# Performance work log

Measured on AMD Instinct MI355X. Metric: run time of the kernel, lower is better.

Reference implementation:

```python
import jax, jax.numpy as jnp
import numpy as np

TOKENS = 512
DIM_HEAD = 64
MAX_TOKENS = 2000
HEADS = 8
BATCH = 8


def _build_indices(tokens: int, max_tokens: int) -> np.ndarray:
    # Faithful replication of the torch index construction (done once in numpy).
    idx = np.arange(-tokens, tokens + 1)
    pad = max_tokens - 2 * tokens + 1
    row = np.concatenate([np.full(pad, idx[0]), idx, np.full(pad, idx[-1])])
    mat = np.stack([np.roll(row, i) for i in range(max_tokens)])
    mat = mat[: max_tokens - tokens + 2, max_tokens - tokens + 1 :]
    # torch fancy indexing wraps negative indices -> take mod of table size
    return (mat % (2 * tokens - 1)).astype(np.int32)


def setup_inputs() -> dict:
    key = jax.random.key(0)
    kq, kp = jax.random.split(key)
    scale = DIM_HEAD ** (-0.5)
    q = jax.random.normal(kq, (BATCH, HEADS, TOKENS, DIM_HEAD), dtype=jnp.float32)
    rel_pos_emb = (
        jax.random.normal(kp, (HEADS, 2 * TOKENS - 1, DIM_HEAD), dtype=jnp.float32)
        * scale
    )
    indices = jnp.asarray(_build_indices(TOKENS, MAX_TOKENS))
    return {"q": q, "rel_pos_emb": rel_pos_emb, "indices": indices}


def reference(q, rel_pos_emb, indices):
    t = q.shape[2]
    idx = indices[:t, :t]  # [r, t]
    # gather: [heads, r, t, dim_head]
    gathered = rel_pos_emb[:, idx]
    # emb[b,h,t,r] = sum_d q[b,h,t,d] * gathered[h,r,t,d]
    return jnp.einsum("bhtd,hrtd->bhtr", q, gathered)
```

## Files before the change

kernel.cpp:

```cpp
#include <hip/hip_runtime.h>


#define TOKENS 512
#define DIMH 64
#define NREL 1023
#define IDXN 1490

#define ESTR 72
#define PSTR 17
#define PCOLS 80

typedef short bf16x8 __attribute__((ext_vector_type(8)));
typedef float f32x4 __attribute__((ext_vector_type(4)));

__device__ __forceinline__ unsigned short f2bf(float x) {
    unsigned u = __float_as_uint(x);
    return (unsigned short)((u + 0x7FFFu + ((u >> 16) & 1u)) >> 16);
}
__device__ __forceinline__ bf16x8 cvt8(float4 a, float4 b) {
    bf16x8 r;
    r[0] = (short)f2bf(a.x); r[1] = (short)f2bf(a.y);
    r[2] = (short)f2bf(a.z); r[3] = (short)f2bf(a.w);
    r[4] = (short)f2bf(b.x); r[5] = (short)f2bf(b.y);
    r[6] = (short)f2bf(b.z); r[7] = (short)f2bf(b.w);
    return r;
}

__global__ __launch_bounds__(256, 4)
void relpos_wave(const float* __restrict__ q,
                 const float* __restrict__ emb,
                 const int* __restrict__ indices,
                 float* __restrict__ out)
{
    __shared__ unsigned short Es[128 * ESTR];
    __shared__ float Ps[4 * PCOLS * PSTR];

    const int tid = threadIdx.x;
    const int blk = blockIdx.x;
    const int rt = blk & 7;
    const int tt = (blk >> 3) & 7;
    const int bh = blk >> 6;
    const int h  = bh & 7;
    const int t0 = tt * 64;
    const int r0 = rt * 64;

    const int j_a = indices[(size_t)(r0 + 63) * IDXN + t0];

    const int lane = tid & 63;
    const int wave = tid >> 6;
    const int quad = lane >> 4;
    const int l15  = lane & 15;

    {
        const float* embh = emb + (size_t)h * NREL * DIMH;
        const int c16 = tid & 15;
        const int rbase = tid >> 4;
#pragma unroll
        for (int it = 0; it < 8; ++it) {
            const int row = rbase + it * 16;
            int j = j_a + row;
            if (j >= NREL) j -= NREL;
            const float4 v = *(const float4*)(embh + (size_t)j * DIMH + c16 * 4);
            ushort4 w = { f2bf(v.x), f2bf(v.y), f2bf(v.z), f2bf(v.w) };
            *(ushort4*)(Es + (size_t)row * ESTR + c16 * 4) = w;
        }
    }

    bf16x8 af0, af1;
    {
        const float* qp = q + ((size_t)bh * TOKENS + t0 + wave * 16 + l15) * DIMH
                        + quad * 8;
        float4 a0 = *(const float4*)qp;
        float4 a1 = *(const float4*)(qp + 4);
        float4 c0 = *(const float4*)(qp + 32);
        float4 c1 = *(const float4*)(qp + 36);
        af0 = cvt8(a0, a1);
        af1 = cvt8(c0, c1);
    }

    __syncthreads();

    float* psw = Ps + (size_t)wave * (PCOLS * PSTR);

#pragma unroll
    for (int i = 0; i < 5; ++i) {
        const unsigned short* bp = Es + (size_t)(wave * 16 + i * 16 + l15) * ESTR
                                 + quad * 8;
        bf16x8 b0 = *(const bf16x8*)bp;
        bf16x8 b1 = *(const bf16x8*)(bp + 32);
        f32x4 acc = {0.f, 0.f, 0.f, 0.f};
        acc = __builtin_amdgcn_mfma_f32_16x16x32_bf16(af0, b0, acc, 0, 0, 0);
        acc = __builtin_amdgcn_mfma_f32_16x16x32_bf16(af1, b1, acc, 0, 0, 0);
        float* pw = psw + (size_t)(i * 16 + l15) * PSTR + quad * 4;
        pw[0] = acc[0]; pw[1] = acc[1]; pw[2] = acc[2]; pw[3] = acc[3];
    }

    const int v16 = l15;
    const int ug  = quad;
    float* ob = out + ((size_t)(bh * TOKENS + t0 + wave * 16)) * TOKENS
              + r0 + v16 * 4;
#pragma unroll
    for (int p = 0; p < 4; ++p) {
        const int u = ug + p * 4;
        const int colbase = u + 63 - v16 * 4;
        float4 o;
        o.x = psw[(size_t)(colbase    ) * PSTR + u];
        o.y = psw[(size_t)(colbase - 1) * PSTR + u];
        o.z = psw[(size_t)(colbase - 2) * PSTR + u];
        o.w = psw[(size_t)(colbase - 3) * PSTR + u];
        *(float4*)(ob + (size_t)u * TOKENS) = o;
    }
}

extern "C" void kernel_launch(void* const* d_in, const int* in_sizes, int n_in,
                              void* d_out, int out_size, void* d_ws, size_t ws_size,
                              hipStream_t stream) {
    const float* q       = (const float*)d_in[0];
    const float* emb     = (const float*)d_in[1];
    const int*   indices = (const int*)d_in[2];
    float* out = (float*)d_out;

    relpos_wave<<<dim3(4096), dim3(256), 0, stream>>>(q, emb, indices, out);
}
```

Measured before the change: 96.76 us.

## Reuse gathered embedding tile across four batches per block with q prefetch

Each block now loops over four batches for the same head and tile, so the gathered and bf16-converted relative-position embedding tile in shared memory is reused instead of being rebuilt for every batch. The grid shrinks accordingly, and the next batch's q rows are prefetched while the current one is computed. The MFMA operand order is swapped so results land transposed and can be written to shared memory as vectors, and conversion uses the HIP bf16 intrinsic. The cost is fewer blocks and a longer serial loop per block.

```diff
diff --git a/kernel.cpp b/kernel.cpp
--- a/kernel.cpp
+++ b/kernel.cpp
@@ -1,4 +1,5 @@
 #include <hip/hip_runtime.h>
+#include <hip/hip_bf16.h>
 
 
 #define TOKENS 512
@@ -7,40 +8,41 @@
 #define IDXN 1490
 
 #define ESTR 72
-#define PSTR 17
-#define PCOLS 80
+#define PSTR 84
 
 typedef short bf16x8 __attribute__((ext_vector_type(8)));
 typedef float f32x4 __attribute__((ext_vector_type(4)));
 
-__device__ __forceinline__ unsigned short f2bf(float x) {
-    unsigned u = __float_as_uint(x);
-    return (unsigned short)((u + 0x7FFFu + ((u >> 16) & 1u)) >> 16);
+__device__ __forceinline__ ushort4 cvt4(float4 v) {
+    union { __hip_bfloat162 h2[2]; ushort4 s; } u;
+    u.h2[0] = __float22bfloat162_rn(float2{v.x, v.y});
+    u.h2[1] = __float22bfloat162_rn(float2{v.z, v.w});
+    return u.s;
 }
 __device__ __forceinline__ bf16x8 cvt8(float4 a, float4 b) {
-    bf16x8 r;
-    r[0] = (short)f2bf(a.x); r[1] = (short)f2bf(a.y);
-    r[2] = (short)f2bf(a.z); r[3] = (short)f2bf(a.w);
-    r[4] = (short)f2bf(b.x); r[5] = (short)f2bf(b.y);
-    r[6] = (short)f2bf(b.z); r[7] = (short)f2bf(b.w);
-    return r;
+    union { __hip_bfloat162 h2[4]; bf16x8 v; } u;
+    u.h2[0] = __float22bfloat162_rn(float2{a.x, a.y});
+    u.h2[1] = __float22bfloat162_rn(float2{a.z, a.w});
+    u.h2[2] = __float22bfloat162_rn(float2{b.x, b.y});
+    u.h2[3] = __float22bfloat162_rn(float2{b.z, b.w});
+    return u.v;
 }
 
 __global__ __launch_bounds__(256, 4)
-void relpos_wave(const float* __restrict__ q,
-                 const float* __restrict__ emb,
-                 const int* __restrict__ indices,
-                 float* __restrict__ out)
+void relpos_batch(const float* __restrict__ q,
+                  const float* __restrict__ emb,
+                  const int* __restrict__ indices,
+                  float* __restrict__ out)
 {
     __shared__ unsigned short Es[128 * ESTR];
-    __shared__ float Ps[4 * PCOLS * PSTR];
+    __shared__ float Ps[4 * 16 * PSTR];
 
     const int tid = threadIdx.x;
     const int blk = blockIdx.x;
     const int rt = blk & 7;
     const int tt = (blk >> 3) & 7;
-    const int bh = blk >> 6;
-    const int h  = bh & 7;
+    const int h  = (blk >> 6) & 7;
+    const int bg = blk >> 9;
     const int t0 = tt * 64;
     const int r0 = rt * 64;
 
@@ -61,54 +63,69 @@
             int j = j_a + row;
             if (j >= NREL) j -= NREL;
             const float4 v = *(const float4*)(embh + (size_t)j * DIMH + c16 * 4);
-            ushort4 w = { f2bf(v.x), f2bf(v.y), f2bf(v.z), f2bf(v.w) };
-            *(ushort4*)(Es + (size_t)row * ESTR + c16 * 4) = w;
+            *(ushort4*)(Es + (size_t)row * ESTR + c16 * 4) = cvt4(v);
         }
     }
 
-    bf16x8 af0, af1;
-    {
-        const float* qp = q + ((size_t)bh * TOKENS + t0 + wave * 16 + l15) * DIMH
-                        + quad * 8;
-        float4 a0 = *(const float4*)qp;
-        float4 a1 = *(const float4*)(qp + 4);
-        float4 c0 = *(const float4*)(qp + 32);
-        float4 c1 = *(const float4*)(qp + 36);
-        af0 = cvt8(a0, a1);
-        af1 = cvt8(c0, c1);
-    }
+    const size_t qstep = (size_t)8 * TOKENS * DIMH;
+    const float* qp = q + ((size_t)(bg * 32 + h) * TOKENS + t0 + wave * 16 + l15) * DIMH
+                    + quad * 8;
+    float4 qa0 = *(const float4*)qp;
+    float4 qa1 = *(const float4*)(qp + 4);
+    float4 qa2 = *(const float4*)(qp + 32);
+    float4 qa3 = *(const float4*)(qp + 36);
 
     __syncthreads();
 
-    float* psw = Ps + (size_t)wave * (PCOLS * PSTR);
-
+    bf16x8 ae[5][2];
 #pragma unroll
     for (int i = 0; i < 5; ++i) {
         const unsigned short* bp = Es + (size_t)(wave * 16 + i * 16 + l15) * ESTR
                                  + quad * 8;
-        bf16x8 b0 = *(const bf16x8*)bp;
-        bf16x8 b1 = *(const bf16x8*)(bp + 32);
-        f32x4 acc = {0.f, 0.f, 0.f, 0.f};
-        acc = __builtin_amdgcn_mfma_f32_16x16x32_bf16(af0, b0, acc, 0, 0, 0);
-        acc = __builtin_amdgcn_mfma_f32_16x16x32_bf16(af1, b1, acc, 0, 0, 0);
-        float* pw = psw + (size_t)(i * 16 + l15) * PSTR + quad * 4;
-        pw[0] = acc[0]; pw[1] = acc[1]; pw[2] = acc[2]; pw[3] = acc[3];
+        ae[i][0] = *(const bf16x8*)bp;
+        ae[i][1] = *(const bf16x8*)(bp + 32);
     }
 
-    const int v16 = l15;
-    const int ug  = quad;
-    float* ob = out + ((size_t)(bh * TOKENS + t0 + wave * 16)) * TOKENS
-              + r0 + v16 * 4;
+    float* psw = Ps + (size_t)wave * 16 * PSTR;
+    float* outw = out + ((size_t)(bg * 32 + h) * TOKENS + t0 + wave * 16) * (size_t)TOKENS
+                + r0 + l15 * 4;
+
 #pragma unroll
-    for (int p = 0; p < 4; ++p) {
-        const int u = ug + p * 4;
-        const int colbase = u + 63 - v16 * 4;
-        float4 o;
-        o.x = psw[(size_t)(colbase    ) * PSTR + u];
-        o.y = psw[(size_t)(colbase - 1) * PSTR + u];
-        o.z = psw[(size_t)(colbase - 2) * PSTR + u];
-        o.w = psw[(size_t)(colbase - 3) * PSTR + u];
-        *(float4*)(ob + (size_t)u * TOKENS) = o;
+    for (int bi = 0; bi < 4; ++bi) {
+        float4 nb0 = qa0, nb1 = qa1, nb2 = qa2, nb3 = qa3;
+        if (bi < 3) {
+            const float* np = qp + qstep * (bi + 1);
+            nb0 = *(const float4*)np;
+            nb1 = *(const float4*)(np + 4);
+            nb2 = *(const float4*)(np + 32);
+            nb3 = *(const float4*)(np + 36);
+        }
+
+        const bf16x8 bq0 = cvt8(qa0, qa1);
+        const bf16x8 bq1 = cvt8(qa2, qa3);
+
+#pragma unroll
+        for (int i = 0; i < 5; ++i) {
+            f32x4 acc = {0.f, 0.f, 0.f, 0.f};
+            acc = __builtin_amdgcn_mfma_f32_16x16x32_bf16(ae[i][0], bq0, acc, 0, 0, 0);
+            acc = __builtin_amdgcn_mfma_f32_16x16x32_bf16(ae[i][1], bq1, acc, 0, 0, 0);
+            *(f32x4*)(psw + (size_t)l15 * PSTR + i * 16 + quad * 4) = acc;
+        }
+
+        float* ob = outw + (size_t)bi * 8 * TOKENS * TOKENS;
+#pragma unroll
+        for (int p = 0; p < 4; ++p) {
+            const int u = quad + p * 4;
+            const float* pr = psw + (size_t)u * PSTR + (u + 63 - l15 * 4);
+            float4 o;
+            o.x = pr[0];
+            o.y = pr[-1];
+            o.z = pr[-2];
+            o.w = pr[-3];
+            *(float4*)(ob + (size_t)u * TOKENS) = o;
+        }
+
+        qa0 = nb0; qa1 = nb1; qa2 = nb2; qa3 = nb3;
     }
 }
 
@@ -120,5 +137,5 @@
     const int*   indices = (const int*)d_in[2];
     float* out = (float*)d_out;
 
-    relpos_wave<<<dim3(4096), dim3(256), 0, stream>>>(q, emb, indices, out);
+    relpos_batch<<<dim3(1024), dim3(256), 0, stream>>>(q, emb, indices, out);
 }
```

After: 98.69 us. About the same (+2.0%).
